# Kernel tuning notes

Measured on AMD Instinct MI355X. Metric: run time of the kernel, lower is better.

## Reference

```python
import jax, jax.numpy as jnp
import numpy as np

HIDDEN = 1024
LAYERS = 2
BATCH = 64
LENGTH = 128


def setup_inputs() -> dict:
    key = jax.random.key(0)
    ks = jax.random.split(key, 7)
    k = 1.0 / np.sqrt(HIDDEN)  # torch default LSTM init scale
    u = lambda kk, shape: jax.random.uniform(kk, shape, jnp.float32, -k, k)
    return {
        "initial_input": jax.random.normal(ks[0], (BATCH, 1, HIDDEN), jnp.float32),
        "h0": jax.random.normal(ks[1], (LAYERS, BATCH, HIDDEN), jnp.float32),
        "c0": jax.random.normal(ks[2], (LAYERS, BATCH, HIDDEN), jnp.float32),
        "W_ih": u(ks[3], (LAYERS, 4 * HIDDEN, HIDDEN)),
        "W_hh": u(ks[4], (LAYERS, 4 * HIDDEN, HIDDEN)),
        "b_ih": u(ks[5], (LAYERS, 4 * HIDDEN)),
        "b_hh": u(ks[6], (LAYERS, 4 * HIDDEN)),
        "length": LENGTH,
    }


def _lstm_step(x, h, c, W_ih, W_hh, b_ih, b_hh):
    """One timestep through all stacked layers.
    x: [B,H]; h,c: [L,B,H]. Returns (top_output, new_h, new_c)."""
    L = h.shape[0]
    new_h, new_c = [], []
    inp = x
    for l in range(L):  # small static layer count
        gates = inp @ W_ih[l].T + h[l] @ W_hh[l].T + b_ih[l] + b_hh[l]  # [B,4H]
        i, f, g, o = jnp.split(gates, 4, axis=-1)  # torch gate order i,f,g,o
        c_l = jax.nn.sigmoid(f) * c[l] + jax.nn.sigmoid(i) * jnp.tanh(g)
        h_l = jax.nn.sigmoid(o) * jnp.tanh(c_l)
        new_h.append(h_l)
        new_c.append(c_l)
        inp = h_l
    return inp, jnp.stack(new_h), jnp.stack(new_c)


def reference(initial_input, h0, c0, W_ih, W_hh, b_ih, b_hh, length):
    x0 = initial_input[:, 0, :]  # [B,H] (seq dim is 1)

    def step(carry, _):
        x, h, c = carry
        out, h, c = _lstm_step(x, h, c, W_ih, W_hh, b_ih, b_hh)
        return (out, h, c), out

    _, ys = jax.lax.scan(step, (x0, h0, c0), None, length=length)  # ys: [T,B,H]
    return jnp.transpose(ys, (1, 0, 2))  # [B,T,H], matches torch.cat(axis=1)
```

## Files before the change

kernel.cpp:

```cpp
#include <hip/hip_runtime.h>
#include <hip/hip_fp16.h>

#define HID   1024
#define NBAT  64
#define NBLK  256
#define NTHR  256
#define AROW  2056
#define AVEC  257
#define PLANE 65536

typedef _Float16 f16;
typedef unsigned long long u64;
typedef __attribute__((ext_vector_type(8))) _Float16 f16x8;
typedef __attribute__((ext_vector_type(4))) float f32x4;

#define A_BYTES   (2 * 16 * AROW * 2)
#define SCR_OFF   A_BYTES
#define C_OFF     (SCR_OFF + 16384)
#define BIAS_OFF  (C_OFF + 2048)
#define HS_OFF    (BIAS_OFF + 128)
#define LDS_BYTES (HS_OFF + 512)

#define BAR_INTS  (64 * 41)

#define COMPILER_FENCE() asm volatile("" ::: "memory")

__device__ __forceinline__ float sigm(float x) { return 1.f / (1.f + __expf(-x)); }
__device__ __forceinline__ float tanh_f(float x) {
  float xc = fminf(fmaxf(x, -10.f), 10.f);
  float e = __expf(2.f * xc);
  return (e - 1.f) / (e + 1.f);
}

__device__ __forceinline__ void st64c(void* p, u64 v) {
  __hip_atomic_store((u64*)p, v, __ATOMIC_RELAXED, __HIP_MEMORY_SCOPE_AGENT);
}

__global__ void bar_init(int* bar) {
  int i = threadIdx.x;
  #pragma unroll
  for (int k = 0; k < 3; ++k) {
    int idx = i + k * 1024;
    if (idx < BAR_INTS) bar[idx] = 0;
  }
}

__global__ __launch_bounds__(NTHR, 1) void lstm_kernel(
    const float* __restrict__ x0, const float* __restrict__ h0,
    const float* __restrict__ c0, const float* __restrict__ Wih,
    const float* __restrict__ Whh, const float* __restrict__ bih,
    const float* __restrict__ bhh, const int* __restrict__ lenp,
    float* __restrict__ out, int* __restrict__ bar, f16* __restrict__ planes)
{
  extern __shared__ char smem[];
  f16*   Alds  = (f16*)smem;
  float* scr   = (float*)(smem + SCR_OFF);
  float* cS    = (float*)(smem + C_OFF);
  float* biasS = (float*)(smem + BIAS_OFF);
  f16*   hS    = (f16*)(smem + HS_OFF);

  const int tid  = threadIdx.x;
  const int blk  = blockIdx.x;
  const int wave = tid >> 6;
  const int lane = tid & 63;
  const int quad = lane >> 4;
  const int l15  = lane & 15;
  const int T    = *lenp;

  f16* l0P[2] = { planes,             planes + PLANE };
  f16* l1P[2] = { planes + 2 * PLANE, planes + 3 * PLANE };
  f16* xP     =   planes + 4 * PLANE;

  const int leafid = blk & 15;
  int* leaf  = bar + 64 * leafid;
  int* relme = bar + 64 * (17 + leafid);

  unsigned xcc;
  asm volatile("s_getreg_b32 %0, hwreg(HW_REG_XCC_ID)" : "=s"(xcc));
  xcc &= 7;
  int is_leader = 0;
  if (tid == 0) {
    int p = __hip_atomic_fetch_add(bar + 64 * (33 + xcc), 1, __ATOMIC_RELAXED,
                                   __HIP_MEMORY_SCOPE_AGENT);
    is_leader = (p == 0);
  }

  {
    int r    = tid >> 2;
    int part = tid & 3;
    int l    = r >> 5;
    int m    = (r >> 1) & 15;
    int half = r & 1;
    int g    = m >> 2, j = m & 3;
    size_t grow = (size_t)g * HID + blk * 4 + j;
    const float* srcW = (half ? Whh : Wih) + ((size_t)l * 4 * HID + grow) * HID + part * 256;
    f16x8* dst = (f16x8*)(Alds + (size_t)(l * 16 + m) * AROW + half * HID + part * 256);
    const float4* s4 = (const float4*)srcW;
    #pragma unroll 4
    for (int i = 0; i < 32; ++i) {
      float4 w0 = s4[2 * i], w1 = s4[2 * i + 1];
      f16x8 o = {(f16)w0.x, (f16)w0.y, (f16)w0.z, (f16)w0.w,
                 (f16)w1.x, (f16)w1.y, (f16)w1.z, (f16)w1.w};
      dst[i] = o;
    }
  }
  if (tid < 32) {
    int l = tid >> 4, m = tid & 15;
    int g = m >> 2, j = m & 3;
    size_t row = (size_t)g * HID + blk * 4 + j;
    biasS[l * 16 + m] = bih[(size_t)l * 4 * HID + row] + bhh[(size_t)l * 4 * HID + row];
  }
  {
    int j = tid >> 6, n = tid & 63;
    #pragma unroll
    for (int l = 0; l < 2; ++l)
      cS[l * 256 + j * 64 + n] =
          c0[(size_t)l * NBAT * HID + (size_t)n * HID + blk * 4 + j];
  }
  if (tid < 128) {
    int l = tid >> 6, n = tid & 63;
    const float* hp = h0 + (size_t)l * NBAT * HID + (size_t)n * HID + blk * 4;
    union { u64 q; f16 h[4]; } pk;
    pk.h[0] = (f16)hp[0]; pk.h[1] = (f16)hp[1]; pk.h[2] = (f16)hp[2]; pk.h[3] = (f16)hp[3];
    st64c((l == 0 ? l0P[1] : l1P[1]) + blk * 256 + n * 4, pk.q);
  }
  if (tid < 64) {
    int n = tid;
    const float* xp = x0 + (size_t)n * HID + blk * 4;
    union { u64 q; f16 h[4]; } pk;
    pk.h[0] = (f16)xp[0]; pk.h[1] = (f16)xp[1]; pk.h[2] = (f16)xp[2]; pk.h[3] = (f16)xp[3];
    st64c(xP + blk * 256 + n * 4, pk.q);
  }
  if (wave == 0) asm volatile("buffer_inv sc1" ::: "memory");

  int epoch = 1;

  #define ARRIVE()                                                              \
    do {                                                                        \
      asm volatile("s_waitcnt vmcnt(0)" ::: "memory");                          \
      if (tid == 0) {                                                           \
        int prev = __hip_atomic_fetch_add(leaf, 1, __ATOMIC_RELAXED,            \
                                          __HIP_MEMORY_SCOPE_AGENT);            \
        if (prev == 16 * epoch - 1) {                                           \
          _Pragma("unroll")                                                     \
          for (int i_ = 0; i_ < 16; ++i_)                                       \
            (void)__hip_atomic_fetch_add(bar + 64 * (17 + i_), 1,               \
                                         __ATOMIC_RELAXED,                      \
                                         __HIP_MEMORY_SCOPE_AGENT);             \
        }                                                                       \
      }                                                                         \
    } while (0)

  #define WAIT_REL()                                                            \
    do {                                                                        \
      if (tid == 0) {                                                           \
        while (__hip_atomic_fetch_add(relme, 0, __ATOMIC_RELAXED,               \
                                      __HIP_MEMORY_SCOPE_AGENT) < 16 * epoch)   \
          __builtin_amdgcn_s_sleep(1);                                          \
      }                                                                         \
      epoch++;                                                                  \
      __syncthreads();                                                          \
      COMPILER_FENCE();                                                         \
    } while (0)

  asm volatile("s_waitcnt vmcnt(0)" ::: "memory");
  __syncthreads();
  ARRIVE();
  WAIT_REL();

  const f16x8* Av = (const f16x8*)Alds;
  const f32x4 fz = {0.f, 0.f, 0.f, 0.f};
  f32x4 a0, a1, a2, a3;

  auto gemmK256 = [&](const f16* psrc, int aoff) {
    const f16* p0 = psrc + (wave * 64 + quad * 2) * 256 + l15 * 4;
    #pragma unroll
    for (int kk = 0; kk < 8; ++kk) {
      f16x8 af = Av[aoff + kk * 4];
      const f16* k0 = p0 + kk * 2048;
      union { u64 q[2]; f16x8 v; } b0, b1, b2, b3;
      b0.q[0] = *(const u64*)(k0 +   0); b0.q[1] = *(const u64*)(k0 + 256);
      b1.q[0] = *(const u64*)(k0 +  64); b1.q[1] = *(const u64*)(k0 + 320);
      b2.q[0] = *(const u64*)(k0 + 128); b2.q[1] = *(const u64*)(k0 + 384);
      b3.q[0] = *(const u64*)(k0 + 192); b3.q[1] = *(const u64*)(k0 + 448);
      a0 = __builtin_amdgcn_mfma_f32_16x16x32_f16(af, b0.v, a0, 0, 0, 0);
      a1 = __builtin_amdgcn_mfma_f32_16x16x32_f16(af, b1.v, a1, 0, 0, 0);
      a2 = __builtin_amdgcn_mfma_f32_16x16x32_f16(af, b2.v, a2, 0, 0, 0);
      a3 = __builtin_amdgcn_mfma_f32_16x16x32_f16(af, b3.v, a3, 0, 0, 0);
    }
  };

  a0 = fz; a1 = fz; a2 = fz; a3 = fz;
  gemmK256(l0P[1], (0 * 16 + l15) * AVEC + 128 + wave * 32 + quad);

  const int NP = 2 * T;
  #pragma unroll 1
  for (int p = 0; p < NP; ++p) {
    const int L = p & 1, t = p >> 1, wp = t & 1, rp = wp ^ 1;
    if (p) WAIT_REL();

    const f16* pIh = L ? l0P[wp] : (t ? l1P[rp] : xP);
    gemmK256(pIh, (L * 16 + l15) * AVEC + wave * 32 + quad);

    float* sc = scr + wave * 1024;
    #pragma unroll
    for (int r = 0; r < 4; ++r) {
      int base = (quad * 4 + r) * 64 + l15;
      sc[base +  0] = a0[r];
      sc[base + 16] = a1[r];
      sc[base + 32] = a2[r];
      sc[base + 48] = a3[r];
    }
    __syncthreads();

    {
      int j = tid >> 6, n = tid & 63;
      float gate[4];
      #pragma unroll
      for (int g = 0; g < 4; ++g) {
        int b0i = (g * 4 + j) * 64 + n;
        gate[g] = scr[b0i] + scr[1024 + b0i] + scr[2048 + b0i] + scr[3072 + b0i]
                + biasS[L * 16 + g * 4 + j];
      }
      float cold = cS[L * 256 + j * 64 + n];
      float cn = sigm(gate[1]) * cold + sigm(gate[0]) * tanh_f(gate[2]);
      float hn = sigm(gate[3]) * tanh_f(cn);
      cS[L * 256 + j * 64 + n] = cn;
      hS[n * 4 + j] = (f16)hn;
    }
    __syncthreads();

    if (tid < 64) {
      int n = tid;
      union { u64 q; f16 h[4]; } pk;
      pk.q = *(const u64*)(hS + n * 4);
      st64c((L == 0 ? l0P[wp] : l1P[wp]) + blk * 256 + n * 4, pk.q);
      if (L == 1) {
        union { u64 q; float f[2]; } o0, o1;
        o0.f[0] = (float)pk.h[0]; o0.f[1] = (float)pk.h[1];
        o1.f[0] = (float)pk.h[2]; o1.f[1] = (float)pk.h[3];
        float* op = out + (size_t)n * T * HID + (size_t)t * HID + blk * 4;
        st64c(op, o0.q);
        st64c(op + 2, o1.q);
      }
    }

    if (p < NP - 1) {
      ARRIVE();
      const f16* pSh = L ? l0P[wp] : l1P[rp];
      a0 = fz; a1 = fz; a2 = fz; a3 = fz;
      gemmK256(pSh, ((L ^ 1) * 16 + l15) * AVEC + 128 + wave * 32 + quad);
      if (is_leader) asm volatile("buffer_inv sc1" ::: "memory");
    } else {
      asm volatile("s_waitcnt vmcnt(0)" ::: "memory");
    }
  }
}

extern "C" void kernel_launch(void* const* d_in, const int* in_sizes, int n_in,
                              void* d_out, int out_size, void* d_ws, size_t ws_size,
                              hipStream_t stream) {
  const float* x0  = (const float*)d_in[0];
  const float* h0  = (const float*)d_in[1];
  const float* c0  = (const float*)d_in[2];
  const float* Wih = (const float*)d_in[3];
  const float* Whh = (const float*)d_in[4];
  const float* bih = (const float*)d_in[5];
  const float* bhh = (const float*)d_in[6];
  const int* lenp  = (const int*)d_in[7];
  float* out = (float*)d_out;

  int* bar    = (int*)d_ws;
  f16* planes = (f16*)((char*)d_ws + 16384);

  hipFuncSetAttribute((const void*)lstm_kernel,
                      hipFuncAttributeMaxDynamicSharedMemorySize, LDS_BYTES);

  bar_init<<<1, 1024, 0, stream>>>(bar);

  void* args[] = {&x0, &h0, &c0, &Wih, &Whh, &bih, &bhh, &lenp, &out, &bar, &planes};
  hipLaunchCooperativeKernel((void*)lstm_kernel, dim3(NBLK), dim3(NTHR),
                             args, LDS_BYTES, stream);
}
```

Before: 1.650 ms.

## Double threads per block and split batch columns across wave pairs

```diff
diff --git a/kernel.cpp b/kernel.cpp
--- a/kernel.cpp
+++ b/kernel.cpp
@@ -4,7 +4,7 @@
 #define HID   1024
 #define NBAT  64
 #define NBLK  256
-#define NTHR  256
+#define NTHR  512
 #define AROW  2056
 #define AVEC  257
 #define PLANE 65536
@@ -65,6 +65,8 @@
   const int lane = tid & 63;
   const int quad = lane >> 4;
   const int l15  = lane & 15;
+  const int kg   = wave >> 1;
+  const int half = wave & 1;
   const int T    = *lenp;
 
   f16* l0P[2] = { planes,             planes + PLANE };
@@ -86,18 +88,18 @@
   }
 
   {
-    int r    = tid >> 2;
-    int part = tid & 3;
+    int r    = tid >> 3;
+    int part = tid & 7;
     int l    = r >> 5;
     int m    = (r >> 1) & 15;
-    int half = r & 1;
+    int hf   = r & 1;
     int g    = m >> 2, j = m & 3;
     size_t grow = (size_t)g * HID + blk * 4 + j;
-    const float* srcW = (half ? Whh : Wih) + ((size_t)l * 4 * HID + grow) * HID + part * 256;
-    f16x8* dst = (f16x8*)(Alds + (size_t)(l * 16 + m) * AROW + half * HID + part * 256);
+    const float* srcW = (hf ? Whh : Wih) + ((size_t)l * 4 * HID + grow) * HID + part * 128;
+    f16x8* dst = (f16x8*)(Alds + (size_t)(l * 16 + m) * AROW + hf * HID + part * 128);
     const float4* s4 = (const float4*)srcW;
     #pragma unroll 4
-    for (int i = 0; i < 32; ++i) {
+    for (int i = 0; i < 16; ++i) {
       float4 w0 = s4[2 * i], w1 = s4[2 * i + 1];
       f16x8 o = {(f16)w0.x, (f16)w0.y, (f16)w0.z, (f16)w0.w,
                  (f16)w1.x, (f16)w1.y, (f16)w1.z, (f16)w1.w};
@@ -110,7 +112,7 @@
     size_t row = (size_t)g * HID + blk * 4 + j;
     biasS[l * 16 + m] = bih[(size_t)l * 4 * HID + row] + bhh[(size_t)l * 4 * HID + row];
   }
-  {
+  if (tid < 256) {
     int j = tid >> 6, n = tid & 63;
     #pragma unroll
     for (int l = 0; l < 2; ++l)
@@ -170,28 +172,25 @@
 
   const f16x8* Av = (const f16x8*)Alds;
   const f32x4 fz = {0.f, 0.f, 0.f, 0.f};
-  f32x4 a0, a1, a2, a3;
-
-  auto gemmK256 = [&](const f16* psrc, int aoff) {
-    const f16* p0 = psrc + (wave * 64 + quad * 2) * 256 + l15 * 4;
+  f32x4 a0, a1;
+
+  auto gemmSlice = [&](const f16* psrc, int aoffbase) {
+    int aoff = aoffbase + kg * 32 + quad;
+    const f16* p0 = psrc + (kg * 64 + quad * 2) * 256 + l15 * 4 + half * 128;
     #pragma unroll
     for (int kk = 0; kk < 8; ++kk) {
       f16x8 af = Av[aoff + kk * 4];
       const f16* k0 = p0 + kk * 2048;
-      union { u64 q[2]; f16x8 v; } b0, b1, b2, b3;
+      union { u64 q[2]; f16x8 v; } b0, b1;
       b0.q[0] = *(const u64*)(k0 +   0); b0.q[1] = *(const u64*)(k0 + 256);
       b1.q[0] = *(const u64*)(k0 +  64); b1.q[1] = *(const u64*)(k0 + 320);
-      b2.q[0] = *(const u64*)(k0 + 128); b2.q[1] = *(const u64*)(k0 + 384);
-      b3.q[0] = *(const u64*)(k0 + 192); b3.q[1] = *(const u64*)(k0 + 448);
       a0 = __builtin_amdgcn_mfma_f32_16x16x32_f16(af, b0.v, a0, 0, 0, 0);
       a1 = __builtin_amdgcn_mfma_f32_16x16x32_f16(af, b1.v, a1, 0, 0, 0);
-      a2 = __builtin_amdgcn_mfma_f32_16x16x32_f16(af, b2.v, a2, 0, 0, 0);
-      a3 = __builtin_amdgcn_mfma_f32_16x16x32_f16(af, b3.v, a3, 0, 0, 0);
     }
   };
 
-  a0 = fz; a1 = fz; a2 = fz; a3 = fz;
-  gemmK256(l0P[1], (0 * 16 + l15) * AVEC + 128 + wave * 32 + quad);
+  a0 = fz; a1 = fz;
+  gemmSlice(l0P[1], (0 * 16 + l15) * AVEC + 128);
 
   const int NP = 2 * T;
   #pragma unroll 1
@@ -200,20 +199,20 @@
     if (p) WAIT_REL();
 
     const f16* pIh = L ? l0P[wp] : (t ? l1P[rp] : xP);
-    gemmK256(pIh, (L * 16 + l15) * AVEC + wave * 32 + quad);
-
-    float* sc = scr + wave * 1024;
-    #pragma unroll
-    for (int r = 0; r < 4; ++r) {
-      int base = (quad * 4 + r) * 64 + l15;
-      sc[base +  0] = a0[r];
-      sc[base + 16] = a1[r];
-      sc[base + 32] = a2[r];
-      sc[base + 48] = a3[r];
+    gemmSlice(pIh, (L * 16 + l15) * AVEC);
+
+    {
+      float* sc = scr + kg * 1024;
+      #pragma unroll
+      for (int r = 0; r < 4; ++r) {
+        int base = (quad * 4 + r) * 64 + l15 + half * 32;
+        sc[base +  0] = a0[r];
+        sc[base + 16] = a1[r];
+      }
     }
     __syncthreads();
 
-    {
+    if (tid < 256) {
       int j = tid >> 6, n = tid & 63;
       float gate[4];
       #pragma unroll
@@ -248,8 +247,8 @@
     if (p < NP - 1) {
       ARRIVE();
       const f16* pSh = L ? l0P[wp] : l1P[rp];
-      a0 = fz; a1 = fz; a2 = fz; a3 = fz;
-      gemmK256(pSh, ((L ^ 1) * 16 + l15) * AVEC + 128 + wave * 32 + quad);
+      a0 = fz; a1 = fz;
+      gemmSlice(pSh, ((L ^ 1) * 16 + l15) * AVEC + 128);
       if (is_leader) asm volatile("buffer_inv sc1" ::: "memory");
     } else {
       asm volatile("s_waitcnt vmcnt(0)" ::: "memory");
```

After: 1.630 ms (median of 2 runs). No clear change (-1.2%).
